# Performance work log

Hardware: AMD Instinct MI355X
Metric: run time of the kernel (lower is better)

The kernel has to match this reference:

```python
import jax, jax.numpy as jnp
import numpy as np
from jax import lax

K = 3          # spline order
G = 5          # grid intervals
R0, R1 = -4.0, 4.0  # grid_range
IN, HID, OUT = 32, 128, 16
BATCH, SEQ = 256, 512


def make_grid(n_in):
    # extended knot vector: G+2K+1 knots per input, uniform spacing h
    h = (R1 - R0) / G
    knots = R0 + h * jnp.arange(-K, G + K + 1, dtype=jnp.float32)  # [G+2K+1]
    return jnp.broadcast_to(knots, (n_in, G + 2 * K + 1))


def b_splines(x, grid):
    # Cox-de Boor recursion. x: [B, n], grid: [n, G+2K+1] -> basis [B, n, G+K]
    xg = x[..., None]
    B = ((xg >= grid[:, :-1]) & (xg < grid[:, 1:])).astype(x.dtype)
    for d in range(1, K + 1):
        B = ((xg - grid[:, :-(d + 1)]) / (grid[:, d:-1] - grid[:, :-(d + 1)]) * B[..., :-1]
             + (grid[:, d + 1:] - xg) / (grid[:, d + 1:] - grid[:, 1:-d]) * B[..., 1:])
    return B


def kan_layer(x, coef, scale_base, scale_sp, grid):
    # y[b,o] = sum_i scale_base[i,o]*silu(x[b,i]) + scale_sp[i,o]*spline_io(x[b,i])
    base = jax.nn.silu(x)                               # [B, n_in]
    Bsp = b_splines(x, grid)                            # [B, n_in, G+K]
    spline = jnp.einsum('bik,iok->bio', Bsp, coef)      # [B, n_in, n_out]
    return (jnp.einsum('bi,io->bo', base, scale_base)
            + jnp.einsum('bio,io->bo', spline, scale_sp))


def setup_inputs() -> dict:
    key = jax.random.key(0)
    ks = jax.random.split(key, 7)
    x = jax.random.normal(ks[0], (BATCH, SEQ, IN), dtype=jnp.float32)
    coef1 = jax.random.normal(ks[1], (IN + HID, HID, G + K), dtype=jnp.float32) * 0.1
    sb1 = jax.random.normal(ks[2], (IN + HID, HID), dtype=jnp.float32) * 0.05
    sp1 = jax.random.normal(ks[3], (IN + HID, HID), dtype=jnp.float32) * 0.05
    coef2 = jax.random.normal(ks[4], (HID, OUT, G + K), dtype=jnp.float32) * 0.1
    sb2 = jax.random.normal(ks[5], (HID, OUT), dtype=jnp.float32) * 0.05
    sp2 = jax.random.normal(ks[6], (HID, OUT), dtype=jnp.float32) * 0.05
    return {"x": x, "coef1": coef1, "sb1": sb1, "sp1": sp1,
            "coef2": coef2, "sb2": sb2, "sp2": sp2}


def reference(x, coef1, sb1, sp1, coef2, sb2, sp2):
    grid1 = make_grid(IN + HID)
    grid2 = make_grid(HID)

    def step(h, x_t):
        combined = jnp.concatenate([x_t, h], axis=1)        # [B, IN+HID]
        h_new = kan_layer(combined, coef1, sb1, sp1, grid1)  # [B, HID]
        out_t = kan_layer(h_new, coef2, sb2, sp2, grid2)     # [B, OUT]
        return h_new, out_t

    h0 = jnp.zeros((x.shape[0], HID), dtype=x.dtype)
    _, outs = lax.scan(step, h0, jnp.swapaxes(x, 0, 1))  # outs: [T, B, OUT]
    # original stacks all timestep outputs then returns outputs[:, -1, :]
    return outs[-1]
```

## Files before the change

### kernel.cpp

```cpp
#include <hip/hip_runtime.h>
#include <hip/hip_bf16.h>

#define NIN 32
#define NHID 128
#define NOUT 16
#define NIN1 160
#define SEQT 512
#define NB 256
#define SEGI 40

#if defined(__has_builtin)
#if __has_builtin(__builtin_amdgcn_fdot2_f32_bf16)
#define HAVE_DOT2BF 1
#endif
#endif
#ifndef HAVE_DOT2BF
#define HAVE_DOT2BF 0
#endif

__device__ __forceinline__ unsigned int f2bfbits(float f) {
    unsigned int u = __float_as_uint(f);
    return (u + 0x7fffu + ((u >> 16) & 1u)) >> 16;
}
__device__ __forceinline__ unsigned int packbf(float lo, float hi) {
    return f2bfbits(lo) | (f2bfbits(hi) << 16);
}

#if HAVE_DOT2BF
typedef __bf16 bf16x2 __attribute__((ext_vector_type(2)));
__device__ __forceinline__ float dot2w(unsigned int a, unsigned int b, float c) {
    return __builtin_amdgcn_fdot2_f32_bf16(__builtin_bit_cast(bf16x2, a),
                                           __builtin_bit_cast(bf16x2, b), c, false);
}
#else
__device__ __forceinline__ float dot2w(unsigned int a, unsigned int b, float c) {
    float alo = __uint_as_float(a << 16), ahi = __uint_as_float(a & 0xffff0000u);
    float blo = __uint_as_float(b << 16), bhi = __uint_as_float(b & 0xffff0000u);
    return __builtin_fmaf(ahi, bhi, __builtin_fmaf(alo, blo, c));
}
#endif

__device__ __forceinline__ void spline_feat(float c, float* out4, int* jst) {
    const float t0 = -8.8f, hh = 1.6f;
    int m0 = (int)floorf((c - t0) / hh);
    bool valid = (m0 >= 0) && (m0 <= 10);
    float v0 = 1.f, v1 = 0.f, v2 = 0.f, v3 = 0.f;
    #pragma unroll
    for (int d = 1; d <= 3; ++d) {
        float inv = 1.f / (d * hh);
        float nv[4];
        float pv[4] = {v0, v1, v2, v3};
        #pragma unroll
        for (int r = 3; r >= 0; --r) {
            if (r > d) { nv[r] = 0.f; continue; }
            int m = m0 - d + r;
            float tm = t0 + hh * (float)m;
            float left  = (r >= 1) ? pv[r-1] : 0.f;
            float right = (r <= d-1) ? pv[r] : 0.f;
            nv[r] = ((c - tm) * left + (tm + hh * (float)(d+1) - c) * right) * inv;
        }
        v0 = nv[0]; v1 = nv[1]; v2 = nv[2]; v3 = nv[3];
    }
    float v[4] = {v0, v1, v2, v3};
    int jb = m0 - 3;
    int js = jb < 0 ? 0 : (jb > 4 ? 4 : jb);
    int sh = js - jb;
    #pragma unroll
    for (int r = 0; r < 4; ++r) {
        int rs = r + sh;
        out4[r] = (valid && rs >= 0 && rs <= 3) ? v[rs] : 0.f;
    }
    *jst = js;
}

__device__ __forceinline__ float fsilu(float c) {
    return c * __builtin_amdgcn_rcpf(1.f + __expf(-c));
}

#define R20(X) X(0) X(1) X(2) X(3) X(4) X(5) X(6) X(7) X(8) X(9) \
               X(10) X(11) X(12) X(13) X(14) X(15) X(16) X(17) X(18) X(19)

__attribute__((amdgpu_waves_per_eu(2, 2)))
__global__ void __launch_bounds__(512)
kan_seq(const float* __restrict__ x,
        const float* __restrict__ coef1,
        const float* __restrict__ sb1,
        const float* __restrict__ sp1,
        const float* __restrict__ coef2,
        const float* __restrict__ sb2,
        const float* __restrict__ sp2,
        float* __restrict__ out)
{
    __shared__ __align__(16) unsigned int Fb[NIN1][4];
    __shared__ float Fsil[NIN1];
    __shared__ float red[4][NHID];
    __shared__ float Hf[NHID][9];

    const int tid  = threadIdx.x;
    const int b    = blockIdx.x;
    const int o    = tid & 127;
    const int seg  = tid >> 7;
    const int i0   = seg * SEGI;
    const int lane = tid & 63;

#define DECLP(p) uint4 wA##p, wB##p; unsigned int sbp##p;
    R20(DECLP)
#undef DECLP

#define INITP(p) { \
    const int iA = i0 + 2 * (p), iB = i0 + 2 * (p) + 1; \
    const float4* ca = (const float4*)(coef1 + (size_t)(iA * NHID + o) * 8); \
    const float4* cb = (const float4*)(coef1 + (size_t)(iB * NHID + o) * 8); \
    float spA = sp1[iA * NHID + o], spB = sp1[iB * NHID + o]; \
    float4 a0 = ca[0], a1 = ca[1], b0v = cb[0], b1v = cb[1]; \
    wA##p = make_uint4(packbf(spA * a0.x, spA * a0.y), packbf(spA * a0.z, spA * a0.w), \
                       packbf(spA * a1.x, spA * a1.y), packbf(spA * a1.z, spA * a1.w)); \
    wB##p = make_uint4(packbf(spB * b0v.x, spB * b0v.y), packbf(spB * b0v.z, spB * b0v.w), \
                       packbf(spB * b1v.x, spB * b1v.y), packbf(spB * b1v.z, spB * b1v.w)); \
    sbp##p = packbf(sb1[iA * NHID + o], sb1[iB * NHID + o]); }
    R20(INITP)
#undef INITP

    ((float*)red)[tid] = 0.f;
    float xv = (tid < NIN) ? x[(size_t)b * SEQT * NIN + tid] : 0.f;
    __syncthreads();

    for (int t = 0; t < SEQT; ++t) {
        if (tid < NIN1) {
            float c;
            if (tid < NIN) c = xv;
            else {
                int hi = tid - NIN;
                c = red[0][hi] + red[1][hi] + red[2][hi] + red[3][hi];
            }
            float sil = fsilu(c);
            float b4[4]; int js;
            spline_feat(c, b4, &js);
            float e[8];
            #pragma unroll
            for (int k = 0; k < 8; ++k) {
                int d = k - js;
                e[k] = (d >= 0 && d < 4) ? b4[d] : 0.f;
            }
            uint4 pk;
            pk.x = packbf(e[0], e[1]); pk.y = packbf(e[2], e[3]);
            pk.z = packbf(e[4], e[5]); pk.w = packbf(e[6], e[7]);
            *(uint4*)&Fb[tid][0] = pk;
            Fsil[tid] = sil;
        }
        if (tid < NIN) {
            int tn = (t + 1 < SEQT) ? (t + 1) : t;
            xv = x[((size_t)b * SEQT + tn) * NIN + tid];
        }
        __syncthreads();

        float vsil = Fsil[i0 + (lane < SEGI ? lane : 0)];
        float ac0 = 0.f, ac1 = 0.f, ac2 = 0.f, ac3 = 0.f;
#define DOTP(p) { \
        float sb_lo = __uint_as_float(sbp##p << 16); \
        float sb_hi = __uint_as_float(sbp##p & 0xffff0000u); \
        float slA = __int_as_float(__builtin_amdgcn_readlane(__float_as_int(vsil), 2 * (p))); \
        float slB = __int_as_float(__builtin_amdgcn_readlane(__float_as_int(vsil), 2 * (p) + 1)); \
        uint4 bA = *(const uint4*)&Fb[i0 + 2 * (p)][0]; \
        uint4 bB = *(const uint4*)&Fb[i0 + 2 * (p) + 1][0]; \
        ac0 = __builtin_fmaf(slA, sb_lo, ac0); \
        ac0 = dot2w(bA.x, wA##p.x, ac0); ac1 = dot2w(bA.y, wA##p.y, ac1); \
        ac2 = dot2w(bA.z, wA##p.z, ac2); ac3 = dot2w(bA.w, wA##p.w, ac3); \
        ac1 = __builtin_fmaf(slB, sb_hi, ac1); \
        ac0 = dot2w(bB.x, wB##p.x, ac0); ac1 = dot2w(bB.y, wB##p.y, ac1); \
        ac2 = dot2w(bB.z, wB##p.z, ac2); ac3 = dot2w(bB.w, wB##p.w, ac3); }
        R20(DOTP)
#undef DOTP
        red[seg][o] = (ac0 + ac1) + (ac2 + ac3);
        __syncthreads();
    }

    if (tid < NHID) {
        float c = red[0][tid] + red[1][tid] + red[2][tid] + red[3][tid];
        float sil = fsilu(c);
        float b4[4]; int js;
        spline_feat(c, b4, &js);
        #pragma unroll
        for (int k = 0; k < 8; ++k) {
            int d = k - js;
            Hf[tid][k] = (d >= 0 && d < 4) ? b4[d] : 0.f;
        }
        Hf[tid][8] = sil;
    }
    __syncthreads();
    if (tid < 128) {
        int o2 = tid & 15, isg = tid >> 4;
        float acc = 0.f;
        for (int q = 0; q < 16; ++q) {
            int i = isg * 16 + q;
            const float* c2 = coef2 + (size_t)(i * NOUT + o2) * 8;
            float s = 0.f;
            #pragma unroll
            for (int k = 0; k < 8; ++k) s += Hf[i][k] * c2[k];
            acc += Hf[i][8] * sb2[i * NOUT + o2] + sp2[i * NOUT + o2] * s;
        }
        ((float*)red)[isg * 16 + o2] = acc;
    }
    __syncthreads();
    if (tid < NOUT) {
        float a = 0.f;
        #pragma unroll
        for (int g = 0; g < 8; ++g) a += ((float*)red)[g * 16 + tid];
        out[(size_t)b * NOUT + tid] = a;
    }
}

extern "C" void kernel_launch(void* const* d_in, const int* in_sizes, int n_in,
                              void* d_out, int out_size, void* d_ws, size_t ws_size,
                              hipStream_t stream) {
    kan_seq<<<NB, 512, 0, stream>>>(
        (const float*)d_in[0], (const float*)d_in[1], (const float*)d_in[2],
        (const float*)d_in[3], (const float*)d_in[4], (const float*)d_in[5],
        (const float*)d_in[6], (float*)d_out);
}
```

Measured before the change: 1.063 ms.

## Broadcast spline features via readlane and split layer-1 weights across registers and LDS

Adds a new kernel that packs each input's eight bf16 spline features plus its SiLU value into one record. Each wave loads its whole segment of records with one or two vector LDS reads and broadcasts per-input values with readlane, replacing the 40 per-input broadcast LDS loads of the old inner loop. Each thread keeps 32 of its 40 inputs' packed weights in registers; the remaining 8 go to shared memory and are read every step. A host-side register-count check picks this kernel or the previous one as a fallback, which adds a driver query to every launch and may cost extra scalar-to-vector latency from the readlanes.

```diff
diff --git a/kernel.cpp b/kernel.cpp
--- a/kernel.cpp
+++ b/kernel.cpp
@@ -7,7 +7,6 @@
 #define NIN1 160
 #define SEQT 512
 #define NB 256
-#define SEGI 40
 
 #if defined(__has_builtin)
 #if __has_builtin(__builtin_amdgcn_fdot2_f32_bf16)
@@ -77,12 +76,26 @@
     return c * __builtin_amdgcn_rcpf(1.f + __expf(-c));
 }
 
-#define R20(X) X(0) X(1) X(2) X(3) X(4) X(5) X(6) X(7) X(8) X(9) \
-               X(10) X(11) X(12) X(13) X(14) X(15) X(16) X(17) X(18) X(19)
-
-__attribute__((amdgpu_waves_per_eu(2, 2)))
-__global__ void __launch_bounds__(512)
-kan_seq(const float* __restrict__ x,
+__device__ __forceinline__ unsigned int RL(unsigned int v, int lane) {
+    return (unsigned int)__builtin_amdgcn_readlane((int)v, lane);
+}
+
+__device__ __forceinline__ void feat_record(float c, uint4* pk, float* sil) {
+    *sil = fsilu(c);
+    float b4[4]; int js;
+    spline_feat(c, b4, &js);
+    float e[8];
+    #pragma unroll
+    for (int k = 0; k < 8; ++k) {
+        int d = k - js;
+        e[k] = (d >= 0 && d < 4) ? b4[d] : 0.f;
+    }
+    pk->x = packbf(e[0], e[1]); pk->y = packbf(e[2], e[3]);
+    pk->z = packbf(e[4], e[5]); pk->w = packbf(e[6], e[7]);
+}
+
+__global__ void __launch_bounds__(512, 2)
+kan_big(const float* __restrict__ x,
         const float* __restrict__ coef1,
         const float* __restrict__ sb1,
         const float* __restrict__ sp1,
@@ -91,6 +104,149 @@
         const float* __restrict__ sp2,
         float* __restrict__ out)
 {
+    __shared__ __align__(16) uint4 WcL[32 * 128];
+    __shared__ float WsbL[32 * 128];
+    __shared__ __align__(16) unsigned int Frec[160 * 8];
+    __shared__ float red[4][NHID];
+    __shared__ float Hf[NHID][9];
+
+    const int tid  = threadIdx.x;
+    const int b    = blockIdx.x;
+    const int o    = tid & 127;
+    const int seg  = tid >> 7;
+    const int lane = tid & 63;
+
+    for (int p = tid; p < 32 * 128; p += 512) {
+        int iL = p >> 7, oo = p & 127;
+        int i = (iL >> 3) * 40 + 32 + (iL & 7);
+        const float4* cp = (const float4*)(coef1 + (size_t)(i * NHID + oo) * 8);
+        float sp = sp1[i * NHID + oo];
+        float4 a = cp[0], c = cp[1];
+        WcL[p] = make_uint4(packbf(sp * a.x, sp * a.y), packbf(sp * a.z, sp * a.w),
+                            packbf(sp * c.x, sp * c.y), packbf(sp * c.z, sp * c.w));
+        WsbL[p] = sb1[i * NHID + oo];
+    }
+    uint4 wc[32];
+    float sbv[32];
+    #pragma unroll
+    for (int r = 0; r < 32; ++r) {
+        int i = seg * 40 + r;
+        const float4* cp = (const float4*)(coef1 + (size_t)(i * NHID + o) * 8);
+        float sp = sp1[i * NHID + o];
+        float4 a = cp[0], c = cp[1];
+        wc[r] = make_uint4(packbf(sp * a.x, sp * a.y), packbf(sp * a.z, sp * a.w),
+                           packbf(sp * c.x, sp * c.y), packbf(sp * c.z, sp * c.w));
+        sbv[r] = sb1[i * NHID + o];
+    }
+
+    ((float*)red)[tid] = 0.f;
+    float xv = (tid < NIN) ? x[(size_t)b * SEQT * NIN + tid] : 0.f;
+    __syncthreads();
+
+    for (int t = 0; t < SEQT; ++t) {
+        if (tid < NIN1) {
+            float c;
+            if (tid < NIN) c = xv;
+            else {
+                int hi = tid - NIN;
+                c = (red[0][hi] + red[1][hi]) + (red[2][hi] + red[3][hi]);
+            }
+            uint4 pk; float sil;
+            feat_record(c, &pk, &sil);
+            unsigned int* R = &Frec[tid * 8];
+            *(uint4*)R = pk;
+            R[4] = __float_as_uint(sil);
+        }
+        if (tid < NIN) {
+            int tn = (t + 1 < SEQT) ? (t + 1) : t;
+            xv = x[((size_t)b * SEQT + tn) * NIN + tid];
+        }
+        __syncthreads();
+
+        const int segbase = seg * 40 * 8;
+        uint4 vA = *(const uint4*)&Frec[segbase + lane * 4];
+        uint4 vB = make_uint4(0, 0, 0, 0);
+        if (lane < 16) vB = *(const uint4*)&Frec[segbase + 256 + lane * 4];
+
+        float ac0 = 0.f, ac1 = 0.f, ac2 = 0.f, ac3 = 0.f;
+        #pragma unroll
+        for (int r = 0; r < 32; ++r) {
+            unsigned int f0 = RL(vA.x, 2 * r), f1 = RL(vA.y, 2 * r);
+            unsigned int f2 = RL(vA.z, 2 * r), f3 = RL(vA.w, 2 * r);
+            float sl = __uint_as_float(RL(vA.x, 2 * r + 1));
+            ac0 = dot2w(f0, wc[r].x, ac0);
+            ac1 = dot2w(f1, wc[r].y, ac1);
+            ac2 = dot2w(f2, wc[r].z, ac2);
+            ac3 = dot2w(f3, wc[r].w, ac3);
+            ac0 = __builtin_fmaf(sl, sbv[r], ac0);
+        }
+        #pragma unroll
+        for (int q = 0; q < 8; ++q) {
+            int iL = seg * 8 + q;
+            uint4 wv = WcL[(iL << 7) + o];
+            float sbw = WsbL[(iL << 7) + o];
+            unsigned int f0 = RL(vB.x, 2 * q), f1 = RL(vB.y, 2 * q);
+            unsigned int f2 = RL(vB.z, 2 * q), f3 = RL(vB.w, 2 * q);
+            float sl = __uint_as_float(RL(vB.x, 2 * q + 1));
+            ac0 = dot2w(f0, wv.x, ac0);
+            ac1 = dot2w(f1, wv.y, ac1);
+            ac2 = dot2w(f2, wv.z, ac2);
+            ac3 = dot2w(f3, wv.w, ac3);
+            ac1 = __builtin_fmaf(sl, sbw, ac1);
+        }
+        red[seg][o] = (ac0 + ac1) + (ac2 + ac3);
+        __syncthreads();
+    }
+
+    if (tid < NHID) {
+        float c = (red[0][tid] + red[1][tid]) + (red[2][tid] + red[3][tid]);
+        float sil = fsilu(c);
+        float b4[4]; int js;
+        spline_feat(c, b4, &js);
+        #pragma unroll
+        for (int k = 0; k < 8; ++k) {
+            int d = k - js;
+            Hf[tid][k] = (d >= 0 && d < 4) ? b4[d] : 0.f;
+        }
+        Hf[tid][8] = sil;
+    }
+    __syncthreads();
+    if (tid < 128) {
+        int o2 = tid & 15, isg = tid >> 4;
+        float acc = 0.f;
+        for (int q = 0; q < 16; ++q) {
+            int i = isg * 16 + q;
+            const float* c2 = coef2 + (size_t)(i * NOUT + o2) * 8;
+            float s = 0.f;
+            #pragma unroll
+            for (int k = 0; k < 8; ++k) s += Hf[i][k] * c2[k];
+            acc += Hf[i][8] * sb2[i * NOUT + o2] + sp2[i * NOUT + o2] * s;
+        }
+        ((float*)red)[isg * 16 + o2] = acc;
+    }
+    __syncthreads();
+    if (tid < NOUT) {
+        float a = 0.f;
+        #pragma unroll
+        for (int g = 0; g < 8; ++g) a += ((float*)red)[g * 16 + tid];
+        out[(size_t)b * NOUT + tid] = a;
+    }
+}
+
+#define SEGI 40
+#define R20(X) X(0) X(1) X(2) X(3) X(4) X(5) X(6) X(7) X(8) X(9) \
+               X(10) X(11) X(12) X(13) X(14) X(15) X(16) X(17) X(18) X(19)
+
+__global__ void __launch_bounds__(512)
+kan_safe(const float* __restrict__ x,
+         const float* __restrict__ coef1,
+         const float* __restrict__ sb1,
+         const float* __restrict__ sp1,
+         const float* __restrict__ coef2,
+         const float* __restrict__ sb2,
+         const float* __restrict__ sp2,
+         float* __restrict__ out)
+{
     __shared__ __align__(16) unsigned int Fb[NIN1][4];
     __shared__ float Fsil[NIN1];
     __shared__ float red[4][NHID];
@@ -106,7 +262,6 @@
 #define DECLP(p) uint4 wA##p, wB##p; unsigned int sbp##p;
     R20(DECLP)
 #undef DECLP
-
 #define INITP(p) { \
     const int iA = i0 + 2 * (p), iB = i0 + 2 * (p) + 1; \
     const float4* ca = (const float4*)(coef1 + (size_t)(iA * NHID + o) * 8); \
@@ -131,20 +286,10 @@
             if (tid < NIN) c = xv;
             else {
                 int hi = tid - NIN;
-                c = red[0][hi] + red[1][hi] + red[2][hi] + red[3][hi];
+                c = (red[0][hi] + red[1][hi]) + (red[2][hi] + red[3][hi]);
             }
-            float sil = fsilu(c);
-            float b4[4]; int js;
-            spline_feat(c, b4, &js);
-            float e[8];
-            #pragma unroll
-            for (int k = 0; k < 8; ++k) {
-                int d = k - js;
-                e[k] = (d >= 0 && d < 4) ? b4[d] : 0.f;
-            }
-            uint4 pk;
-            pk.x = packbf(e[0], e[1]); pk.y = packbf(e[2], e[3]);
-            pk.z = packbf(e[4], e[5]); pk.w = packbf(e[6], e[7]);
+            uint4 pk; float sil;
+            feat_record(c, &pk, &sil);
             *(uint4*)&Fb[tid][0] = pk;
             Fsil[tid] = sil;
         }
@@ -176,7 +321,7 @@
     }
 
     if (tid < NHID) {
-        float c = red[0][tid] + red[1][tid] + red[2][tid] + red[3][tid];
+        float c = (red[0][tid] + red[1][tid]) + (red[2][tid] + red[3][tid]);
         float sil = fsilu(c);
         float b4[4]; int js;
         spline_feat(c, b4, &js);
@@ -213,8 +358,21 @@
 extern "C" void kernel_launch(void* const* d_in, const int* in_sizes, int n_in,
                               void* d_out, int out_size, void* d_ws, size_t ws_size,
                               hipStream_t stream) {
-    kan_seq<<<NB, 512, 0, stream>>>(
-        (const float*)d_in[0], (const float*)d_in[1], (const float*)d_in[2],
-        (const float*)d_in[3], (const float*)d_in[4], (const float*)d_in[5],
-        (const float*)d_in[6], (float*)d_out);
-}
+    const float* x     = (const float*)d_in[0];
+    const float* coef1 = (const float*)d_in[1];
+    const float* sb1   = (const float*)d_in[2];
+    const float* sp1   = (const float*)d_in[3];
+    const float* coef2 = (const float*)d_in[4];
+    const float* sb2   = (const float*)d_in[5];
+    const float* sp2   = (const float*)d_in[6];
+    float* outp = (float*)d_out;
+
+    hipFuncAttributes attr;
+    hipError_t e = hipFuncGetAttributes(&attr, reinterpret_cast<const void*>(kan_big));
+    bool use_big = (e == hipSuccess) && (attr.numRegs >= 160);
+
+    if (use_big)
+        kan_big<<<NB, 512, 0, stream>>>(x, coef1, sb1, sp1, coef2, sb2, sp2, outp);
+    else
+        kan_safe<<<NB, 512, 0, stream>>>(x, coef1, sb1, sp1, coef2, sb2, sp2, outp);
+}
```

After: 1.236 ms. +16.3%, slower.
